# Optimization experiments

Measured on AMD Instinct MI355X. Metric: run time of the kernel, lower is better.

## Reference

```python
import jax, jax.numpy as jnp
import numpy as np

N_NODES = 100000
N_EDGES = 1200000
IN_CH = 64
HID_CH = 64
OUT_CH = 64
N_REL = 5
N_CLS = 8


def setup_inputs() -> dict:
    key = jax.random.key(0)
    ks = jax.random.split(key, 12)
    x = jax.random.normal(ks[0], (N_NODES, IN_CH), dtype=jnp.float32)
    edge_index = jax.random.randint(ks[1], (2, N_EDGES), 0, N_NODES, dtype=jnp.int64)
    edge_type = jax.random.randint(ks[2], (N_EDGES,), 0, N_REL, dtype=jnp.int64)
    s1 = 1.0 / np.sqrt(IN_CH)
    s2 = 1.0 / np.sqrt(HID_CH)
    s3 = 1.0 / np.sqrt(OUT_CH)
    W1 = jax.random.uniform(ks[3], (N_REL, IN_CH, HID_CH), jnp.float32, -s1, s1)
    root1 = jax.random.uniform(ks[4], (IN_CH, HID_CH), jnp.float32, -s1, s1)
    b1 = jax.random.uniform(ks[5], (HID_CH,), jnp.float32, -s1, s1)
    W2 = jax.random.uniform(ks[6], (N_REL, HID_CH, OUT_CH), jnp.float32, -s2, s2)
    root2 = jax.random.uniform(ks[7], (HID_CH, OUT_CH), jnp.float32, -s2, s2)
    b2 = jax.random.uniform(ks[8], (OUT_CH,), jnp.float32, -s2, s2)
    Wc = jax.random.uniform(ks[9], (OUT_CH, N_CLS), jnp.float32, -s3, s3)
    bc = jax.random.uniform(ks[10], (N_CLS,), jnp.float32, -s3, s3)
    return {"x": x, "edge_index": edge_index, "edge_type": edge_type,
            "W1": W1, "root1": root1, "b1": b1,
            "W2": W2, "root2": root2, "b2": b2,
            "Wc": Wc, "bc": bc}


def _rgcn_conv(x, src, dst, edge_type, W, root, bias):
    # PyG RGCNConv (no bases, aggr='mean', root_weight=True, bias=True):
    # out[i] = x[i] @ root + bias + sum_r mean_{(j->i) in rel r} x[j] @ W[r]
    n = x.shape[0]
    out = x @ root + bias
    xs = x[src]  # [E, d] gather once, reused across relations
    for r in range(N_REL):
        w = (edge_type == r).astype(x.dtype)  # [E]
        msg_sum = jax.ops.segment_sum(xs * w[:, None], dst, num_segments=n)  # [N, d]
        cnt = jax.ops.segment_sum(w, dst, num_segments=n)                    # [N]
        agg = msg_sum / jnp.maximum(cnt, 1.0)[:, None]
        out = out + agg @ W[r]
    return out


def reference(x, edge_index, edge_type, W1, root1, b1, W2, root2, b2, Wc, bc):
    src, dst = edge_index[0], edge_index[1]
    h = _rgcn_conv(x, src, dst, edge_type, W1, root1, b1)
    h = jax.nn.relu(h)
    h = _rgcn_conv(h, src, dst, edge_type, W2, root2, b2)
    logits = h @ Wc + bc
    return (h, logits)
```

## Files before the change

### kernel.cpp

```cpp
#include <hip/hip_runtime.h>

#define NN 100000
#define NE 1200000
#define CH 64
#define NREL 5
#define NCLS 8
#define SLOT 64
#define KTOT 384
#define HPAD 66

typedef _Float16 f16;
typedef _Float16 f16x4 __attribute__((ext_vector_type(4)));
typedef _Float16 f16x8 __attribute__((ext_vector_type(8)));
typedef float f32x4 __attribute__((ext_vector_type(4)));

#define RFL __builtin_amdgcn_readfirstlane

__global__ __launch_bounds__(256) void cvt_f16_kernel(const float* __restrict__ x,
                                                      f16* __restrict__ xh) {
    int t = blockIdx.x * 256 + threadIdx.x;
    if (t >= NN * CH / 4) return;
    float4 v = reinterpret_cast<const float4*>(x)[t];
    f16x4 h = {(f16)v.x, (f16)v.y, (f16)v.z, (f16)v.w};
    *reinterpret_cast<f16x4*>(xh + (size_t)t * 4) = h;
}

__global__ __launch_bounds__(256) void scatter_kernel(const int* __restrict__ src,
                                                      const int* __restrict__ dst,
                                                      const int* __restrict__ et,
                                                      int* __restrict__ cursor,
                                                      int* __restrict__ sorted) {
    int e = blockIdx.x * 256 + threadIdx.x;
    if (e >= NE) return;
    int d = dst[e];
    int pos = atomicAdd(&cursor[d], 1);
    if (pos < SLOT) sorted[(size_t)d * SLOT + pos] = src[e] | (et[e] << 17);
}

__global__ __launch_bounds__(256) void prep_weights(const float* __restrict__ root1,
                                                    const float* __restrict__ W1,
                                                    const float* __restrict__ root2,
                                                    const float* __restrict__ W2,
                                                    f16* __restrict__ Btg) {
    int o = blockIdx.x * 256 + threadIdx.x;
    if (o >= 2 * 64 * KTOT) return;
    int layer = o / (64 * KTOT);
    int rem = o % (64 * KTOT);
    int n = rem / KTOT, k = rem % KTOT;
    const float* R = layer ? root2 : root1;
    const float* W = layer ? W2 : W1;
    float v = (k < CH) ? R[k * CH + n] : W[(size_t)(k - CH) * CH + n];
    Btg[o] = (f16)v;
}

template<bool CLS>
__global__ __launch_bounds__(256, 8) void fused_layer2(
    const f16* __restrict__ in, const f16* __restrict__ Btg,
    const float* __restrict__ bias,
    const int* __restrict__ cursor, const int* __restrict__ sorted,
    float* __restrict__ outf, f16* __restrict__ outh,
    const float* __restrict__ Wc, const float* __restrict__ bc,
    float* __restrict__ logits) {
    __shared__ __align__(16) char smem[16 * 784];
    f16* Ap = (f16*)smem;

    const int tid = threadIdx.x;
    const int wv = tid >> 6, lane = tid & 63;
    const int nb0 = blockIdx.x * 16;

    for (int q = 0; q < 4; ++q) {
        int nl = wv * 4 + q;
        int i = nb0 + nl;
        f16* arow = Ap + nl * 392;
        if (i >= NN) {
#pragma unroll
            for (int m = 0; m < 6; ++m) arow[m * 64 + lane] = (f16)0.f;
            continue;
        }
        int deg = cursor[i];
        if (deg > SLOT) deg = SLOT;
        const int* sp = sorted + (size_t)i * SLOT;

        float self = (float)in[(size_t)i * CH + lane];
        float a0 = 0.f, a1 = 0.f, a2 = 0.f, a3 = 0.f, a4 = 0.f;
        int c0 = 0, c1 = 0, c2 = 0, c3 = 0, c4 = 0;

        if (deg > 0) {
            int4 pka = *(const int4*)sp;
            int4 pkb = *(const int4*)(sp + 4);
            for (int e0 = 0; e0 < deg; e0 += 8) {
                int4 nxa = *(const int4*)(sp + e0 + 8);
                int4 nxb = *(const int4*)(sp + e0 + 12);
                int p0 = RFL(pka.x), p1 = RFL(pka.y), p2 = RFL(pka.z), p3 = RFL(pka.w);
                int p4 = RFL(pkb.x), p5 = RFL(pkb.y), p6 = RFL(pkb.z), p7 = RFL(pkb.w);
                uint s0 = (e0 + 0 < deg) ? ((uint)p0 & 0x1FFFF) : (uint)i;
                uint s1 = (e0 + 1 < deg) ? ((uint)p1 & 0x1FFFF) : (uint)i;
                uint s2 = (e0 + 2 < deg) ? ((uint)p2 & 0x1FFFF) : (uint)i;
                uint s3 = (e0 + 3 < deg) ? ((uint)p3 & 0x1FFFF) : (uint)i;
                uint s4 = (e0 + 4 < deg) ? ((uint)p4 & 0x1FFFF) : (uint)i;
                uint s5 = (e0 + 5 < deg) ? ((uint)p5 & 0x1FFFF) : (uint)i;
                uint s6 = (e0 + 6 < deg) ? ((uint)p6 & 0x1FFFF) : (uint)i;
                uint s7 = (e0 + 7 < deg) ? ((uint)p7 & 0x1FFFF) : (uint)i;
                float v0 = (float)in[(size_t)s0 * CH + lane];
                float v1 = (float)in[(size_t)s1 * CH + lane];
                float v2 = (float)in[(size_t)s2 * CH + lane];
                float v3 = (float)in[(size_t)s3 * CH + lane];
                float v4 = (float)in[(size_t)s4 * CH + lane];
                float v5 = (float)in[(size_t)s5 * CH + lane];
                float v6 = (float)in[(size_t)s6 * CH + lane];
                float v7 = (float)in[(size_t)s7 * CH + lane];
#define LAD(J, PJ, VJ)                                                          \
                if (e0 + J < deg) {                                             \
                    int r = (PJ) >> 17;                                         \
                    if (r == 0)      { a0 += (VJ); c0++; }                      \
                    else if (r == 1) { a1 += (VJ); c1++; }                      \
                    else if (r == 2) { a2 += (VJ); c2++; }                      \
                    else if (r == 3) { a3 += (VJ); c3++; }                      \
                    else             { a4 += (VJ); c4++; }                      \
                }
                LAD(0, p0, v0) LAD(1, p1, v1) LAD(2, p2, v2) LAD(3, p3, v3)
                LAD(4, p4, v4) LAD(5, p5, v5) LAD(6, p6, v6) LAD(7, p7, v7)
#undef LAD
                pka = nxa; pkb = nxb;
            }
        }

        float i0 = 1.0f / (float)(c0 > 0 ? c0 : 1);
        float i1 = 1.0f / (float)(c1 > 0 ? c1 : 1);
        float i2 = 1.0f / (float)(c2 > 0 ? c2 : 1);
        float i3 = 1.0f / (float)(c3 > 0 ? c3 : 1);
        float i4 = 1.0f / (float)(c4 > 0 ? c4 : 1);

        arow[0 * 64 + lane] = (f16)self;
        arow[1 * 64 + lane] = (f16)(a0 * i0);
        arow[2 * 64 + lane] = (f16)(a1 * i1);
        arow[3 * 64 + lane] = (f16)(a2 * i2);
        arow[4 * 64 + lane] = (f16)(a3 * i3);
        arow[5 * 64 + lane] = (f16)(a4 * i4);
    }
    __syncthreads();

    const int col = lane & 15, lg = lane >> 4;
    float bv = bias[wv * 16 + col];
    f32x4 acc = {bv, bv, bv, bv};
    const char* Ab = (const char*)Ap + col * 784 + lg * 16;
    const char* Bb = (const char*)Btg + (size_t)(wv * 16 + col) * 768 + lg * 16;
#pragma unroll
    for (int k = 0; k < KTOT / 32; ++k) {
        f16x8 af = *(const f16x8*)(Ab + k * 64);
        f16x8 bf = *(const f16x8*)(Bb + k * 64);
        acc = __builtin_amdgcn_mfma_f32_16x16x32_f16(af, bf, acc, 0, 0, 0);
    }

    if (!CLS) {
#pragma unroll
        for (int r = 0; r < 4; ++r) {
            int node = nb0 + lg * 4 + r;
            if (node < NN)
                outh[(size_t)node * CH + wv * 16 + col] = (f16)fmaxf(acc[r], 0.f);
        }
    } else {
        __syncthreads();
        float* hst = (float*)smem;
#pragma unroll
        for (int r = 0; r < 4; ++r) {
            int nl = lg * 4 + r;
            int node = nb0 + nl;
            hst[nl * HPAD + wv * 16 + col] = acc[r];
            if (node < NN)
                outf[(size_t)node * CH + wv * 16 + col] = acc[r];
        }
        __syncthreads();
        float wcr[NCLS];
#pragma unroll
        for (int c = 0; c < NCLS; ++c) wcr[c] = Wc[lane * NCLS + c];
        for (int q = 0; q < 4; ++q) {
            int nl = wv * 4 + q;
            int i = nb0 + nl;
            if (i >= NN) continue;
            float v = hst[nl * HPAD + lane];
            float p[NCLS];
#pragma unroll
            for (int c = 0; c < NCLS; ++c) p[c] = v * wcr[c];
#pragma unroll
            for (int off = 32; off > 0; off >>= 1) {
#pragma unroll
                for (int c = 0; c < NCLS; ++c) p[c] += __shfl_xor(p[c], off);
            }
            if (lane == 0) {
                float4 lo = make_float4(p[0] + bc[0], p[1] + bc[1], p[2] + bc[2], p[3] + bc[3]);
                float4 hi = make_float4(p[4] + bc[4], p[5] + bc[5], p[6] + bc[6], p[7] + bc[7]);
                *reinterpret_cast<float4*>(&logits[(size_t)i * NCLS]) = lo;
                *reinterpret_cast<float4*>(&logits[(size_t)i * NCLS + 4]) = hi;
            }
        }
    }
}

extern "C" void kernel_launch(void* const* d_in, const int* in_sizes, int n_in,
                              void* d_out, int out_size, void* d_ws, size_t ws_size,
                              hipStream_t stream) {
    const float* x     = (const float*)d_in[0];
    const int*   ei    = (const int*)d_in[1];
    const int*   et    = (const int*)d_in[2];
    const float* W1    = (const float*)d_in[3];
    const float* root1 = (const float*)d_in[4];
    const float* b1    = (const float*)d_in[5];
    const float* W2    = (const float*)d_in[6];
    const float* root2 = (const float*)d_in[7];
    const float* b2    = (const float*)d_in[8];
    const float* Wc    = (const float*)d_in[9];
    const float* bc    = (const float*)d_in[10];
    const int* src = ei;
    const int* dst = ei + NE;

    float* h2     = (float*)d_out;
    float* logits = h2 + (size_t)NN * CH;

    int* cursor = (int*)d_ws;
    int* sorted = cursor + NN;
    f16* h1h    = (f16*)(sorted + (size_t)NN * SLOT + 16);
    f16* xh     = h1h + (size_t)NN * CH;
    f16* Btg    = xh + (size_t)NN * CH;

    (void)hipMemsetAsync(cursor, 0, (size_t)NN * 4, stream);
    cvt_f16_kernel<<<(NN * CH / 4 + 255) / 256, 256, 0, stream>>>(x, xh);
    scatter_kernel<<<(NE + 255) / 256, 256, 0, stream>>>(src, dst, et, cursor, sorted);
    prep_weights<<<(2 * 64 * KTOT + 255) / 256, 256, 0, stream>>>(root1, W1, root2, W2, Btg);

    int nBlk = (NN + 15) / 16;
    fused_layer2<false><<<nBlk, 256, 0, stream>>>(
        xh, Btg, b1, cursor, sorted, nullptr, h1h, nullptr, nullptr, nullptr);
    fused_layer2<true><<<nBlk, 256, 0, stream>>>(
        h1h, Btg + (size_t)64 * KTOT, b2, cursor, sorted, h2, nullptr, Wc, bc, logits);
}
```

Before: 295.4 us.

## Sort neighbor lists by relation and gather two edges per wave

Adds a kernel that uses wave ballots to reorder each node's neighbor slot list by relation type, so consecutive edges usually share a relation. The aggregation loop then processes two edges per wave, with each half-wave loading a packed f16x2 of one source row, and accumulates in half precision with a final cross-half shuffle. This halves gather instructions and branch divergence per edge, at the cost of an extra pass over the sorted adjacency and lower accumulation precision (f16 sums instead of f32).

New measurement: 331.7 us. +12.3%, slower.

```diff
diff --git a/kernel.cpp b/kernel.cpp
--- a/kernel.cpp
+++ b/kernel.cpp
@@ -10,6 +10,7 @@
 #define HPAD 66
 
 typedef _Float16 f16;
+typedef _Float16 f16x2 __attribute__((ext_vector_type(2)));
 typedef _Float16 f16x4 __attribute__((ext_vector_type(4)));
 typedef _Float16 f16x8 __attribute__((ext_vector_type(8)));
 typedef float f32x4 __attribute__((ext_vector_type(4)));
@@ -35,6 +36,33 @@
     int d = dst[e];
     int pos = atomicAdd(&cursor[d], 1);
     if (pos < SLOT) sorted[(size_t)d * SLOT + pos] = src[e] | (et[e] << 17);
+}
+
+__global__ __launch_bounds__(256, 8) void sort_rel(const int* __restrict__ cursor,
+                                                   int* __restrict__ sorted) {
+    int wv = threadIdx.x >> 6;
+    int node = blockIdx.x * 4 + RFL(wv);
+    if (node >= NN) return;
+    int lane = threadIdx.x & 63;
+    int deg = cursor[node];
+    if (deg > SLOT) deg = SLOT;
+    int w = sorted[(size_t)node * SLOT + lane];
+    uint r = (uint)w >> 17;
+    bool valid = lane < deg;
+    unsigned long long b0 = __ballot(valid && r == 0);
+    unsigned long long b1 = __ballot(valid && r == 1);
+    unsigned long long b2 = __ballot(valid && r == 2);
+    unsigned long long b3 = __ballot(valid && r == 3);
+    unsigned long long b4 = __ballot(valid && r == 4);
+    int st1 = (int)__popcll(b0);
+    int st2 = st1 + (int)__popcll(b1);
+    int st3 = st2 + (int)__popcll(b2);
+    int st4 = st3 + (int)__popcll(b3);
+    unsigned long long below = (1ull << lane) - 1ull;
+    unsigned long long br = (r == 0) ? b0 : (r == 1) ? b1 : (r == 2) ? b2 : (r == 3) ? b3 : b4;
+    int str = (r == 0) ? 0 : (r == 1) ? st1 : (r == 2) ? st2 : (r == 3) ? st3 : st4;
+    int pos = str + (int)__popcll(br & below);
+    if (valid) sorted[(size_t)node * SLOT + pos] = w;
 }
 
 __global__ __launch_bounds__(256) void prep_weights(const float* __restrict__ root1,
@@ -66,10 +94,52 @@
 
     const int tid = threadIdx.x;
     const int wv = tid >> 6, lane = tid & 63;
+    const int wvu = RFL(wv);
+    const int ch2 = lane & 31;
+    const bool lo32 = lane < 32;
     const int nb0 = blockIdx.x * 16;
+    const f16x2 hz2 = {(f16)0.f, (f16)0.f};
+
+#define LADP(RS, HV, INC)                                              \
+    if ((RS) == 0)      { A0 += (HV); c0 += (INC); }                   \
+    else if ((RS) == 1) { A1 += (HV); c1 += (INC); }                   \
+    else if ((RS) == 2) { A2 += (HV); c2 += (INC); }                   \
+    else if ((RS) == 3) { A3 += (HV); c3 += (INC); }                   \
+    else                { A4 += (HV); c4 += (INC); }
+
+#define PAIR(WA, WB, E0) {                                             \
+    int w0 = RFL(WA);                                                  \
+    int w1 = RFL(WB);                                                  \
+    bool full = ((E0) + 1 < deg);                                      \
+    if (!full) w1 = w0;                                                \
+    uint r0 = (uint)w0 >> 17, r1 = (uint)w1 >> 17;                     \
+    uint b0a = ((uint)w0 & 0x1FFFF) * 128u + (uint)ch2 * 4u;           \
+    uint b1a = ((uint)w1 & 0x1FFFF) * 128u + (uint)ch2 * 4u;           \
+    uint off = lo32 ? b0a : b1a;                                       \
+    uint vv = *(const uint*)((const char*)in + off);                   \
+    if (!full) vv = lo32 ? vv : 0u;                                    \
+    f16x2 hv = __builtin_bit_cast(f16x2, vv);                          \
+    if (r0 == r1) { int inc = full ? 2 : 1; LADP(r0, hv, inc) }        \
+    else {                                                             \
+        f16x2 hva = lo32 ? hv : hz2;                                   \
+        f16x2 hvb = lo32 ? hz2 : hv;                                   \
+        LADP(r0, hva, 1)                                               \
+        LADP(r1, hvb, 1)                                               \
+    }                                                                  \
+}
+
+#define MST(AV, SC, M) {                                               \
+    int _ai = __builtin_bit_cast(int, AV);                             \
+    int _bi = __shfl_xor(_ai, 32);                                     \
+    f16x2 _t = AV + __builtin_bit_cast(f16x2, _bi);                    \
+    if (lo32) {                                                        \
+        f16x2 _o = {(f16)((float)_t.x * (SC)), (f16)((float)_t.y * (SC))}; \
+        *(uint*)((char*)arow + (M) * 128 + ch2 * 4) = __builtin_bit_cast(uint, _o); \
+    }                                                                  \
+}
 
     for (int q = 0; q < 4; ++q) {
-        int nl = wv * 4 + q;
+        int nl = wvu * 4 + q;
         int i = nb0 + nl;
         f16* arow = Ap + nl * 392;
         if (i >= NN) {
@@ -81,70 +151,39 @@
         if (deg > SLOT) deg = SLOT;
         const int* sp = sorted + (size_t)i * SLOT;
 
-        float self = (float)in[(size_t)i * CH + lane];
-        float a0 = 0.f, a1 = 0.f, a2 = 0.f, a3 = 0.f, a4 = 0.f;
+        f16 sv = in[(size_t)i * CH + lane];
+        f16x2 A0 = hz2, A1 = hz2, A2 = hz2, A3 = hz2, A4 = hz2;
         int c0 = 0, c1 = 0, c2 = 0, c3 = 0, c4 = 0;
 
         if (deg > 0) {
-            int4 pka = *(const int4*)sp;
-            int4 pkb = *(const int4*)(sp + 4);
-            for (int e0 = 0; e0 < deg; e0 += 8) {
-                int4 nxa = *(const int4*)(sp + e0 + 8);
-                int4 nxb = *(const int4*)(sp + e0 + 12);
-                int p0 = RFL(pka.x), p1 = RFL(pka.y), p2 = RFL(pka.z), p3 = RFL(pka.w);
-                int p4 = RFL(pkb.x), p5 = RFL(pkb.y), p6 = RFL(pkb.z), p7 = RFL(pkb.w);
-                uint s0 = (e0 + 0 < deg) ? ((uint)p0 & 0x1FFFF) : (uint)i;
-                uint s1 = (e0 + 1 < deg) ? ((uint)p1 & 0x1FFFF) : (uint)i;
-                uint s2 = (e0 + 2 < deg) ? ((uint)p2 & 0x1FFFF) : (uint)i;
-                uint s3 = (e0 + 3 < deg) ? ((uint)p3 & 0x1FFFF) : (uint)i;
-                uint s4 = (e0 + 4 < deg) ? ((uint)p4 & 0x1FFFF) : (uint)i;
-                uint s5 = (e0 + 5 < deg) ? ((uint)p5 & 0x1FFFF) : (uint)i;
-                uint s6 = (e0 + 6 < deg) ? ((uint)p6 & 0x1FFFF) : (uint)i;
-                uint s7 = (e0 + 7 < deg) ? ((uint)p7 & 0x1FFFF) : (uint)i;
-                float v0 = (float)in[(size_t)s0 * CH + lane];
-                float v1 = (float)in[(size_t)s1 * CH + lane];
-                float v2 = (float)in[(size_t)s2 * CH + lane];
-                float v3 = (float)in[(size_t)s3 * CH + lane];
-                float v4 = (float)in[(size_t)s4 * CH + lane];
-                float v5 = (float)in[(size_t)s5 * CH + lane];
-                float v6 = (float)in[(size_t)s6 * CH + lane];
-                float v7 = (float)in[(size_t)s7 * CH + lane];
-#define LAD(J, PJ, VJ)                                                          \
-                if (e0 + J < deg) {                                             \
-                    int r = (PJ) >> 17;                                         \
-                    if (r == 0)      { a0 += (VJ); c0++; }                      \
-                    else if (r == 1) { a1 += (VJ); c1++; }                      \
-                    else if (r == 2) { a2 += (VJ); c2++; }                      \
-                    else if (r == 3) { a3 += (VJ); c3++; }                      \
-                    else             { a4 += (VJ); c4++; }                      \
-                }
-                LAD(0, p0, v0) LAD(1, p1, v1) LAD(2, p2, v2) LAD(3, p3, v3)
-                LAD(4, p4, v4) LAD(5, p5, v5) LAD(6, p6, v6) LAD(7, p7, v7)
-#undef LAD
-                pka = nxa; pkb = nxb;
+            int npairs = (deg + 1) >> 1;
+            int4 pk = *(const int4*)sp;
+            for (int p0 = 0; p0 < npairs; p0 += 2) {
+                int4 nx = *(const int4*)(sp + 2 * p0 + 4);
+                PAIR(pk.x, pk.y, 2 * p0)
+                if (p0 + 1 < npairs) PAIR(pk.z, pk.w, 2 * p0 + 2)
+                pk = nx;
             }
         }
 
-        float i0 = 1.0f / (float)(c0 > 0 ? c0 : 1);
-        float i1 = 1.0f / (float)(c1 > 0 ? c1 : 1);
-        float i2 = 1.0f / (float)(c2 > 0 ? c2 : 1);
-        float i3 = 1.0f / (float)(c3 > 0 ? c3 : 1);
-        float i4 = 1.0f / (float)(c4 > 0 ? c4 : 1);
-
-        arow[0 * 64 + lane] = (f16)self;
-        arow[1 * 64 + lane] = (f16)(a0 * i0);
-        arow[2 * 64 + lane] = (f16)(a1 * i1);
-        arow[3 * 64 + lane] = (f16)(a2 * i2);
-        arow[4 * 64 + lane] = (f16)(a3 * i3);
-        arow[5 * 64 + lane] = (f16)(a4 * i4);
+        arow[lane] = sv;
+        float s0 = 1.0f / (float)(c0 > 0 ? c0 : 1);
+        float s1 = 1.0f / (float)(c1 > 0 ? c1 : 1);
+        float s2 = 1.0f / (float)(c2 > 0 ? c2 : 1);
+        float s3 = 1.0f / (float)(c3 > 0 ? c3 : 1);
+        float s4 = 1.0f / (float)(c4 > 0 ? c4 : 1);
+        MST(A0, s0, 1) MST(A1, s1, 2) MST(A2, s2, 3) MST(A3, s3, 4) MST(A4, s4, 5)
     }
+#undef PAIR
+#undef LADP
+#undef MST
     __syncthreads();
 
     const int col = lane & 15, lg = lane >> 4;
-    float bv = bias[wv * 16 + col];
+    float bv = bias[wvu * 16 + col];
     f32x4 acc = {bv, bv, bv, bv};
     const char* Ab = (const char*)Ap + col * 784 + lg * 16;
-    const char* Bb = (const char*)Btg + (size_t)(wv * 16 + col) * 768 + lg * 16;
+    const char* Bb = (const char*)Btg + (size_t)(wvu * 16 + col) * 768 + lg * 16;
 #pragma unroll
     for (int k = 0; k < KTOT / 32; ++k) {
         f16x8 af = *(const f16x8*)(Ab + k * 64);
@@ -157,7 +196,7 @@
         for (int r = 0; r < 4; ++r) {
             int node = nb0 + lg * 4 + r;
             if (node < NN)
-                outh[(size_t)node * CH + wv * 16 + col] = (f16)fmaxf(acc[r], 0.f);
+                outh[(size_t)node * CH + wvu * 16 + col] = (f16)fmaxf(acc[r], 0.f);
         }
     } else {
         __syncthreads();
@@ -166,16 +205,16 @@
         for (int r = 0; r < 4; ++r) {
             int nl = lg * 4 + r;
             int node = nb0 + nl;
-            hst[nl * HPAD + wv * 16 + col] = acc[r];
+            hst[nl * HPAD + wvu * 16 + col] = acc[r];
             if (node < NN)
-                outf[(size_t)node * CH + wv * 16 + col] = acc[r];
+                outf[(size_t)node * CH + wvu * 16 + col] = acc[r];
         }
         __syncthreads();
         float wcr[NCLS];
 #pragma unroll
         for (int c = 0; c < NCLS; ++c) wcr[c] = Wc[lane * NCLS + c];
         for (int q = 0; q < 4; ++q) {
-            int nl = wv * 4 + q;
+            int nl = wvu * 4 + q;
             int i = nb0 + nl;
             if (i >= NN) continue;
             float v = hst[nl * HPAD + lane];
@@ -226,6 +265,7 @@
     (void)hipMemsetAsync(cursor, 0, (size_t)NN * 4, stream);
     cvt_f16_kernel<<<(NN * CH / 4 + 255) / 256, 256, 0, stream>>>(x, xh);
     scatter_kernel<<<(NE + 255) / 256, 256, 0, stream>>>(src, dst, et, cursor, sorted);
+    sort_rel<<<(NN + 3) / 4, 256, 0, stream>>>(cursor, sorted);
     prep_weights<<<(2 * 64 * KTOT + 255) / 256, 256, 0, stream>>>(root1, W1, root2, W2, Btg);
 
     int nBlk = (NN + 15) / 16;
```

## Merge convert and scatter kernels, unroll neighbor gather to 16 edges

Applied to the files above, without the earlier changes.

Merges the fp16 conversion and edge-scatter kernels into one launch, splitting the grid by block index, so one kernel boundary disappears and the two independent jobs can overlap. The gather loop now issues 16 neighbor loads per iteration instead of 8 and drops the software-prefetch of packed indices, trading more outstanding memory requests for higher register pressure. The wave index is made uniform with readfirstlane so address arithmetic can use scalar registers.

New measurement: 310.4 us. +5.1%, slower.

```diff
diff --git a/kernel.cpp b/kernel.cpp
--- a/kernel.cpp
+++ b/kernel.cpp
@@ -16,25 +16,24 @@
 
 #define RFL __builtin_amdgcn_readfirstlane
 
-__global__ __launch_bounds__(256) void cvt_f16_kernel(const float* __restrict__ x,
-                                                      f16* __restrict__ xh) {
-    int t = blockIdx.x * 256 + threadIdx.x;
-    if (t >= NN * CH / 4) return;
-    float4 v = reinterpret_cast<const float4*>(x)[t];
-    f16x4 h = {(f16)v.x, (f16)v.y, (f16)v.z, (f16)v.w};
-    *reinterpret_cast<f16x4*>(xh + (size_t)t * 4) = h;
-}
-
-__global__ __launch_bounds__(256) void scatter_kernel(const int* __restrict__ src,
-                                                      const int* __restrict__ dst,
-                                                      const int* __restrict__ et,
-                                                      int* __restrict__ cursor,
-                                                      int* __restrict__ sorted) {
-    int e = blockIdx.x * 256 + threadIdx.x;
-    if (e >= NE) return;
-    int d = dst[e];
-    int pos = atomicAdd(&cursor[d], 1);
-    if (pos < SLOT) sorted[(size_t)d * SLOT + pos] = src[e] | (et[e] << 17);
+__global__ __launch_bounds__(256) void cvt_scatter_kernel(
+    const float* __restrict__ x, f16* __restrict__ xh,
+    const int* __restrict__ src, const int* __restrict__ dst,
+    const int* __restrict__ et, int* __restrict__ cursor,
+    int* __restrict__ sorted, int cvtB) {
+    if ((int)blockIdx.x < cvtB) {
+        int t = blockIdx.x * 256 + threadIdx.x;
+        if (t >= NN * CH / 4) return;
+        float4 v = reinterpret_cast<const float4*>(x)[t];
+        f16x4 h = {(f16)v.x, (f16)v.y, (f16)v.z, (f16)v.w};
+        *reinterpret_cast<f16x4*>(xh + (size_t)t * 4) = h;
+    } else {
+        int e = (blockIdx.x - cvtB) * 256 + threadIdx.x;
+        if (e >= NE) return;
+        int d = dst[e];
+        int pos = atomicAdd(&cursor[d], 1);
+        if (pos < SLOT) sorted[(size_t)d * SLOT + pos] = src[e] | (et[e] << 17);
+    }
 }
 
 __global__ __launch_bounds__(256) void prep_weights(const float* __restrict__ root1,
@@ -66,10 +65,11 @@
 
     const int tid = threadIdx.x;
     const int wv = tid >> 6, lane = tid & 63;
+    const int wvu = RFL(wv);
     const int nb0 = blockIdx.x * 16;
 
     for (int q = 0; q < 4; ++q) {
-        int nl = wv * 4 + q;
+        int nl = wvu * 4 + q;
         int i = nb0 + nl;
         f16* arow = Ap + nl * 392;
         if (i >= NN) {
@@ -85,44 +85,51 @@
         float a0 = 0.f, a1 = 0.f, a2 = 0.f, a3 = 0.f, a4 = 0.f;
         int c0 = 0, c1 = 0, c2 = 0, c3 = 0, c4 = 0;
 
-        if (deg > 0) {
-            int4 pka = *(const int4*)sp;
-            int4 pkb = *(const int4*)(sp + 4);
-            for (int e0 = 0; e0 < deg; e0 += 8) {
-                int4 nxa = *(const int4*)(sp + e0 + 8);
-                int4 nxb = *(const int4*)(sp + e0 + 12);
-                int p0 = RFL(pka.x), p1 = RFL(pka.y), p2 = RFL(pka.z), p3 = RFL(pka.w);
-                int p4 = RFL(pkb.x), p5 = RFL(pkb.y), p6 = RFL(pkb.z), p7 = RFL(pkb.w);
-                uint s0 = (e0 + 0 < deg) ? ((uint)p0 & 0x1FFFF) : (uint)i;
-                uint s1 = (e0 + 1 < deg) ? ((uint)p1 & 0x1FFFF) : (uint)i;
-                uint s2 = (e0 + 2 < deg) ? ((uint)p2 & 0x1FFFF) : (uint)i;
-                uint s3 = (e0 + 3 < deg) ? ((uint)p3 & 0x1FFFF) : (uint)i;
-                uint s4 = (e0 + 4 < deg) ? ((uint)p4 & 0x1FFFF) : (uint)i;
-                uint s5 = (e0 + 5 < deg) ? ((uint)p5 & 0x1FFFF) : (uint)i;
-                uint s6 = (e0 + 6 < deg) ? ((uint)p6 & 0x1FFFF) : (uint)i;
-                uint s7 = (e0 + 7 < deg) ? ((uint)p7 & 0x1FFFF) : (uint)i;
-                float v0 = (float)in[(size_t)s0 * CH + lane];
-                float v1 = (float)in[(size_t)s1 * CH + lane];
-                float v2 = (float)in[(size_t)s2 * CH + lane];
-                float v3 = (float)in[(size_t)s3 * CH + lane];
-                float v4 = (float)in[(size_t)s4 * CH + lane];
-                float v5 = (float)in[(size_t)s5 * CH + lane];
-                float v6 = (float)in[(size_t)s6 * CH + lane];
-                float v7 = (float)in[(size_t)s7 * CH + lane];
+        for (int e0 = 0; e0 < deg; e0 += 16) {
+            int4 pka = *(const int4*)(sp + e0);
+            int4 pkb = *(const int4*)(sp + e0 + 4);
+            int4 pkc = *(const int4*)(sp + e0 + 8);
+            int4 pkd = *(const int4*)(sp + e0 + 12);
+            int p0 = RFL(pka.x), p1 = RFL(pka.y), p2 = RFL(pka.z), p3 = RFL(pka.w);
+            int p4 = RFL(pkb.x), p5 = RFL(pkb.y), p6 = RFL(pkb.z), p7 = RFL(pkb.w);
+            int p8 = RFL(pkc.x), p9 = RFL(pkc.y), pA = RFL(pkc.z), pB = RFL(pkc.w);
+            int pC = RFL(pkd.x), pD = RFL(pkd.y), pE = RFL(pkd.z), pF = RFL(pkd.w);
+#define SIDX(J, PJ) uint s##J = (e0 + 0x##J < deg) ? ((uint)(PJ) & 0x1FFFF) : (uint)i;
+            SIDX(0, p0) SIDX(1, p1) SIDX(2, p2) SIDX(3, p3)
+            SIDX(4, p4) SIDX(5, p5) SIDX(6, p6) SIDX(7, p7)
+            SIDX(8, p8) SIDX(9, p9) SIDX(A, pA) SIDX(B, pB)
+            SIDX(C, pC) SIDX(D, pD) SIDX(E, pE) SIDX(F, pF)
+#undef SIDX
+            float v0 = (float)in[(size_t)s0 * CH + lane];
+            float v1 = (float)in[(size_t)s1 * CH + lane];
+            float v2 = (float)in[(size_t)s2 * CH + lane];
+            float v3 = (float)in[(size_t)s3 * CH + lane];
+            float v4 = (float)in[(size_t)s4 * CH + lane];
+            float v5 = (float)in[(size_t)s5 * CH + lane];
+            float v6 = (float)in[(size_t)s6 * CH + lane];
+            float v7 = (float)in[(size_t)s7 * CH + lane];
+            float v8 = (float)in[(size_t)s8 * CH + lane];
+            float v9 = (float)in[(size_t)s9 * CH + lane];
+            float vA = (float)in[(size_t)sA * CH + lane];
+            float vB = (float)in[(size_t)sB * CH + lane];
+            float vC = (float)in[(size_t)sC * CH + lane];
+            float vD = (float)in[(size_t)sD * CH + lane];
+            float vE = (float)in[(size_t)sE * CH + lane];
+            float vF = (float)in[(size_t)sF * CH + lane];
 #define LAD(J, PJ, VJ)                                                          \
-                if (e0 + J < deg) {                                             \
-                    int r = (PJ) >> 17;                                         \
-                    if (r == 0)      { a0 += (VJ); c0++; }                      \
-                    else if (r == 1) { a1 += (VJ); c1++; }                      \
-                    else if (r == 2) { a2 += (VJ); c2++; }                      \
-                    else if (r == 3) { a3 += (VJ); c3++; }                      \
-                    else             { a4 += (VJ); c4++; }                      \
-                }
-                LAD(0, p0, v0) LAD(1, p1, v1) LAD(2, p2, v2) LAD(3, p3, v3)
-                LAD(4, p4, v4) LAD(5, p5, v5) LAD(6, p6, v6) LAD(7, p7, v7)
+            if (e0 + 0x##J < deg) {                                             \
+                int r = (PJ) >> 17;                                             \
+                if (r == 0)      { a0 += (VJ); c0++; }                          \
+                else if (r == 1) { a1 += (VJ); c1++; }                          \
+                else if (r == 2) { a2 += (VJ); c2++; }                          \
+                else if (r == 3) { a3 += (VJ); c3++; }                          \
+                else             { a4 += (VJ); c4++; }                          \
+            }
+            LAD(0, p0, v0) LAD(1, p1, v1) LAD(2, p2, v2) LAD(3, p3, v3)
+            LAD(4, p4, v4) LAD(5, p5, v5) LAD(6, p6, v6) LAD(7, p7, v7)
+            LAD(8, p8, v8) LAD(9, p9, v9) LAD(A, pA, vA) LAD(B, pB, vB)
+            LAD(C, pC, vC) LAD(D, pD, vD) LAD(E, pE, vE) LAD(F, pF, vF)
 #undef LAD
-                pka = nxa; pkb = nxb;
-            }
         }
 
         float i0 = 1.0f / (float)(c0 > 0 ? c0 : 1);
@@ -141,10 +148,10 @@
     __syncthreads();
 
     const int col = lane & 15, lg = lane >> 4;
-    float bv = bias[wv * 16 + col];
+    float bv = bias[wvu * 16 + col];
     f32x4 acc = {bv, bv, bv, bv};
     const char* Ab = (const char*)Ap + col * 784 + lg * 16;
-    const char* Bb = (const char*)Btg + (size_t)(wv * 16 + col) * 768 + lg * 16;
+    const char* Bb = (const char*)Btg + (size_t)(wvu * 16 + col) * 768 + lg * 16;
 #pragma unroll
     for (int k = 0; k < KTOT / 32; ++k) {
         f16x8 af = *(const f16x8*)(Ab + k * 64);
@@ -157,7 +164,7 @@
         for (int r = 0; r < 4; ++r) {
             int node = nb0 + lg * 4 + r;
             if (node < NN)
-                outh[(size_t)node * CH + wv * 16 + col] = (f16)fmaxf(acc[r], 0.f);
+                outh[(size_t)node * CH + wvu * 16 + col] = (f16)fmaxf(acc[r], 0.f);
         }
     } else {
         __syncthreads();
@@ -166,16 +173,16 @@
         for (int r = 0; r < 4; ++r) {
             int nl = lg * 4 + r;
             int node = nb0 + nl;
-            hst[nl * HPAD + wv * 16 + col] = acc[r];
+            hst[nl * HPAD + wvu * 16 + col] = acc[r];
             if (node < NN)
-                outf[(size_t)node * CH + wv * 16 + col] = acc[r];
+                outf[(size_t)node * CH + wvu * 16 + col] = acc[r];
         }
         __syncthreads();
         float wcr[NCLS];
 #pragma unroll
         for (int c = 0; c < NCLS; ++c) wcr[c] = Wc[lane * NCLS + c];
         for (int q = 0; q < 4; ++q) {
-            int nl = wv * 4 + q;
+            int nl = wvu * 4 + q;
             int i = nb0 + nl;
             if (i >= NN) continue;
             float v = hst[nl * HPAD + lane];
@@ -224,8 +231,9 @@
     f16* Btg    = xh + (size_t)NN * CH;
 
     (void)hipMemsetAsync(cursor, 0, (size_t)NN * 4, stream);
-    cvt_f16_kernel<<<(NN * CH / 4 + 255) / 256, 256, 0, stream>>>(x, xh);
-    scatter_kernel<<<(NE + 255) / 256, 256, 0, stream>>>(src, dst, et, cursor, sorted);
+    int cvtB = (NN * CH / 4 + 255) / 256;
+    int sctB = (NE + 255) / 256;
+    cvt_scatter_kernel<<<cvtB + sctB, 256, 0, stream>>>(x, xh, src, dst, et, cursor, sorted, cvtB);
     prep_weights<<<(2 * 64 * KTOT + 255) / 256, 256, 0, stream>>>(root1, W1, root2, W2, Btg);
 
     int nBlk = (NN + 15) / 16;
```
